# Kernel optimization log

Measured on AMD Instinct MI355X. Metric: run time of the kernel, lower is better.

## Reference

```python
import jax, jax.numpy as jnp
import numpy as np

B, C_IN, C_OUT, H, W = 64, 1024, 1024, 16, 16
HEADS, C_RED = 8, 512  # reduced_ch = 1024 // 2
N = H * W
EPS = 1e-5  # BatchNorm eps (eval mode, running stats)
NEG_SLOPE = 0.2  # PyG GATConv default leaky_relu slope


def build_grid_edge_index(P, Pw):
    # 4-neighbor grid + one self-loop per node, directed [2, E]
    edges = []
    for i in range(P):
        for j in range(Pw):
            u = i * Pw + j
            if i - 1 >= 0: edges.append([u, u - Pw])
            if i + 1 < P:  edges.append([u, u + Pw])
            if j - 1 >= 0: edges.append([u, u - 1])
            if j + 1 < Pw: edges.append([u, u + 1])
            edges.append([u, u])
    return jnp.asarray(np.array(edges, dtype=np.int32).T)


def setup_inputs() -> dict:
    key = jax.random.key(0)
    ks = jax.random.split(key, 10)
    x = jax.random.normal(ks[0], (B, C_IN, H, W), jnp.float32)
    w_reduce = jax.random.normal(ks[1], (C_RED, C_IN), jnp.float32) * 0.02
    g_red = jnp.ones((C_RED,), jnp.float32); b_red = jnp.zeros((C_RED,), jnp.float32)
    m_red = jax.random.normal(ks[2], (C_RED,), jnp.float32) * 0.1
    v_red = jax.random.uniform(ks[3], (C_RED,), jnp.float32) + 0.5
    w_gat = jax.random.normal(ks[4], (C_RED, HEADS * C_RED), jnp.float32) * 0.02
    att_src = jax.random.normal(ks[5], (HEADS, C_RED), jnp.float32) * 0.1
    att_dst = jax.random.normal(ks[6], (HEADS, C_RED), jnp.float32) * 0.1
    gat_bias = jnp.zeros((C_RED,), jnp.float32)
    w_restore = jax.random.normal(ks[7], (C_OUT, C_RED), jnp.float32) * 0.02
    g_res = jnp.ones((C_OUT,), jnp.float32); b_res = jnp.zeros((C_OUT,), jnp.float32)
    m_res = jax.random.normal(ks[8], (C_OUT,), jnp.float32) * 0.1
    v_res = jax.random.uniform(ks[9], (C_OUT,), jnp.float32) + 0.5
    edge_index = build_grid_edge_index(H, W)
    return dict(x=x, w_reduce=w_reduce, g_red=g_red, b_red=b_red, m_red=m_red, v_red=v_red,
                w_gat=w_gat, att_src=att_src, att_dst=att_dst, gat_bias=gat_bias,
                w_restore=w_restore, g_res=g_res, b_res=b_res, m_res=m_res, v_res=v_res,
                edge_index=edge_index)


def _bn(x, g, b, m, v):  # channel-last, eval mode
    return (x - m) * (g * jax.lax.rsqrt(v + EPS)) + b


def reference(x, w_reduce, g_red, b_red, m_red, v_red, w_gat, att_src, att_dst,
              gat_bias, w_restore, g_res, b_res, m_res, v_res, edge_index):
    xh = jnp.transpose(x, (0, 2, 3, 1))                 # [B,H,W,C_in] NHWC
    res = xh                                            # identity residual (C_in == C_out)
    xr = jax.nn.relu(_bn(xh @ w_reduce.T, g_red, b_red, m_red, v_red))  # [B,H,W,C_red]
    nodes = xr.reshape(B, N, C_RED)                     # per-sample grid graph nodes

    # --- GATConv (heads=HEADS, concat=False), batched over B ---
    xp = (nodes @ w_gat).reshape(B, N, HEADS, C_RED)    # projected per-head features
    a_src = jnp.einsum('bnhc,hc->bnh', xp, att_src)
    a_dst = jnp.einsum('bnhc,hc->bnh', xp, att_dst)
    src, dst = edge_index[0], edge_index[1]
    logits = jax.nn.leaky_relu(a_src[:, src] + a_dst[:, dst], NEG_SLOPE)  # [B,E,HEADS]
    seg_max = jax.vmap(lambda a: jax.ops.segment_max(a, dst, num_segments=N))(logits)
    e = jnp.exp(logits - seg_max[:, dst])
    seg_sum = jax.vmap(lambda a: jax.ops.segment_sum(a, dst, num_segments=N))(e)
    alpha = e / seg_sum[:, dst]                          # softmax over incoming edges
    msg = alpha[..., None] * xp[:, src]                  # [B,E,HEADS,C_red]
    agg = jax.vmap(lambda m_: jax.ops.segment_sum(m_, dst, num_segments=N))(msg)
    gat_out = agg.mean(axis=2) + gat_bias                # concat=False -> head mean, [B,N,C_red]

    out = gat_out.reshape(B, H, W, C_RED) @ w_restore.T  # 1x1 restore conv
    out = _bn(out, g_res, b_res, m_res, v_res)
    out = jax.nn.relu(out + res)
    return jnp.transpose(out, (0, 3, 1, 2))              # [B,C_out,H,W]
```

## Files before the change

### kernel.cpp

```cpp
#include <hip/hip_runtime.h>


typedef unsigned short u16;
typedef __attribute__((ext_vector_type(4))) unsigned short u16x4;
typedef __attribute__((ext_vector_type(8))) unsigned short u16x8;
typedef __attribute__((ext_vector_type(8))) __bf16 bf16x8;
typedef __attribute__((ext_vector_type(2))) __bf16 bf16x2;
typedef __attribute__((ext_vector_type(4))) float f32x4;

#if defined(__has_builtin)
#if __has_builtin(__builtin_amdgcn_fdot2_f32_bf16)
#define HAVE_DOT2 1
#endif
#endif

#define B_    64
#define CIN   1024
#define CRED  512
#define COUT  1024
#define NPIX  256
#define HEADS 8
#define KGAT  4096
#define MTOT  16384
#define EPSB  1e-5f

__device__ __forceinline__ float b2f(u16 u) {
  union { unsigned u; float f; } c; c.u = ((unsigned)u) << 16; return c.f;
}
__device__ __forceinline__ u16 f2b(float f) {
  union { float f; unsigned u; } c; c.f = f;
  unsigned r = (c.u + 0x7FFFu + ((c.u >> 16) & 1u)) >> 16;
  return (u16)r;
}

__device__ __forceinline__ void gload_lds16(const void* g, void* lds) {
  __builtin_amdgcn_global_load_lds(
      (const __attribute__((address_space(1))) void*)g,
      (__attribute__((address_space(3))) void*)lds, 16, 0, 0);
}

union U8u {
  u16x8 v;
  bf16x2 p[4];
};

__global__ __launch_bounds__(256) void alphapre_kernel(
    const float* __restrict__ a_all, u16* __restrict__ alf_g)
{
  const int nh = blockIdx.x * 256 + threadIdx.x;
  const int ng = nh >> 3, h = nh & 7;
  const int n = ng & 255;
  const size_t nbase = (size_t)(ng >> 8) * NPIX;
  const int gi = n >> 4, gj = n & 15;
  int vv[5];
  vv[0] = n;
  vv[1] = (gi > 0)  ? n - 16 : -1;
  vv[2] = (gi < 15) ? n + 16 : -1;
  vv[3] = (gj > 0)  ? n - 1  : -1;
  vv[4] = (gj < 15) ? n + 1  : -1;
  const float* a_src = a_all;
  const float* a_dst = a_all + (size_t)MTOT * HEADS;
  const float ad = a_dst[(nbase + n) * HEADS + h];
  float l[5]; float mx = -1e30f;
#pragma unroll
  for (int e = 0; e < 5; ++e) {
    if (vv[e] >= 0) {
      const float xx = a_src[(nbase + vv[e]) * HEADS + h] + ad;
      l[e] = xx > 0.f ? xx : 0.2f * xx;
      mx = fmaxf(mx, l[e]);
    } else l[e] = -1e30f;
  }
  float s = 0.f, ee[5];
#pragma unroll
  for (int e = 0; e < 5; ++e) {
    ee[e] = (vv[e] >= 0) ? __expf(l[e] - mx) : 0.f;
    s += ee[e];
  }
  const float inv = 0.125f / s;
#pragma unroll
  for (int e = 0; e < 5; ++e)
    alf_g[(size_t)ng * 40 + e * 8 + h] = f2b(ee[e] * inv);
}

__global__ __launch_bounds__(512, 4) void gemmf2_kernel(
    const u16* __restrict__ A, const u16* __restrict__ Btp,
    const u16* __restrict__ alf_g, const float* __restrict__ gat_bias,
    u16* __restrict__ gat)
{
  extern __shared__ u16 lds[];
  u16* Ys = lds;

  const int tid = threadIdx.x;
  const int wave = tid >> 6, lane = tid & 63;
  const int wm = wave >> 1, wn = wave & 1;
  const int l15 = lane & 15, l4 = lane >> 4;

  const int raw = blockIdx.x;
  const int lin = (raw & 7) * 256 + (raw >> 3);
  const int img = lin >> 5;
  const int ntile = lin & 31;
  const int n0 = ntile * 128;
  const int jbg = ntile * 16;
  const size_t nbase = (size_t)img * NPIX;

  int offA[2], dstA[2];
#pragma unroll
  for (int i = 0; i < 2; ++i) {
    const int f = i * 512 + tid;
    const int r = f >> 2;
    const int kb = (f & 3) ^ ((r >> 1) & 3);
    offA[i] = r * 512 + kb * 8;
    dstA[i] = (i * 512 + wave * 64) * 8;
  }
  const int rB = tid >> 2;
  const int kbB = (tid & 3) ^ ((rB >> 1) & 3);
  const int offB = rB * 512 + kbB * 8;
  const int dstB = wave * 64 * 8;

  const u16* gA = A + (size_t)img * 256 * 512;
  const u16* gB = Btp + (size_t)n0 * 512;

  auto stage = [&](int t) {
    const int d = (t & 1) * 12288;
    gload_lds16(gA + t * 32 + offA[0], &lds[d + dstA[0]]);
    gload_lds16(gA + t * 32 + offA[1], &lds[d + dstA[1]]);
    gload_lds16(gB + t * 32 + offB, &lds[d + 8192 + dstB]);
  };

  f32x4 acc[4][4];
#pragma unroll
  for (int i = 0; i < 4; ++i)
#pragma unroll
    for (int j = 0; j < 4; ++j) acc[i][j] = f32x4{0.f, 0.f, 0.f, 0.f};

  const int kq = (l4 ^ ((l15 >> 1) & 3)) * 8;
  const int aBase = (wm * 64 + l15) * 32 + kq;
  const int bBase = 8192 + (wn * 64 + l15) * 32 + kq;

  stage(0);

  for (int t = 0; t < 16; ++t) {
    asm volatile("s_waitcnt vmcnt(0)" ::: "memory");
    __builtin_amdgcn_s_barrier();
    const int d = (t & 1) * 12288;
    bf16x8 af[4], bfr[4];
#pragma unroll
    for (int f = 0; f < 4; ++f) {
      af[f]  = *(const bf16x8*)&lds[d + aBase + f * 512];
      bfr[f] = *(const bf16x8*)&lds[d + bBase + f * 512];
    }
    if (t < 15) stage(t + 1);
    __builtin_amdgcn_s_setprio(1);
#pragma unroll
    for (int fm = 0; fm < 4; ++fm)
#pragma unroll
      for (int fn = 0; fn < 4; ++fn)
        acc[fm][fn] = __builtin_amdgcn_mfma_f32_16x16x32_bf16(
            bfr[fn], af[fm], acc[fm][fn], 0, 0, 0);
    __builtin_amdgcn_s_setprio(0);
  }
  __syncthreads();

#pragma unroll
  for (int fm = 0; fm < 4; ++fm) {
    const int nloc = wm * 64 + fm * 16 + l15;
#pragma unroll
    for (int fn = 0; fn < 4; ++fn) {
      const int cloc = wn * 64 + fn * 16 + l4 * 4;
      u16x4 ov;
#pragma unroll
      for (int r = 0; r < 4; ++r) ov[r] = f2b(acc[fm][fn][r]);
      *(u16x4*)&Ys[nloc * 136 + cloc] = ov;
    }
  }
  __syncthreads();

  const int n = tid >> 1, half = tid & 1;
  const int gi = n >> 4, gj = n & 15;
  int vv[5];
  vv[0] = n;
  vv[1] = (gi > 0)  ? n - 16 : n;
  vv[2] = (gi < 15) ? n + 16 : n;
  vv[3] = (gj > 0)  ? n - 1  : n;
  vv[4] = (gj < 15) ? n + 1  : n;
  U8u au[5];
  {
    const u16* ag = alf_g + (nbase + n) * 40;
#pragma unroll
    for (int e = 0; e < 5; ++e) au[e].v = *(const u16x8*)&ag[e * 8];
  }
  float o[8];
  {
    const int jb = jbg + half * 8;
    const float4 b0 = *(const float4*)&gat_bias[jb];
    const float4 b1 = *(const float4*)&gat_bias[jb + 4];
    o[0] = b0.x; o[1] = b0.y; o[2] = b0.z; o[3] = b0.w;
    o[4] = b1.x; o[5] = b1.y; o[6] = b1.z; o[7] = b1.w;
  }
#pragma unroll
  for (int e = 0; e < 5; ++e) {
    const u16* yrow = &Ys[vv[e] * 136 + half * 64];
#if defined(HAVE_DOT2)
#pragma unroll
    for (int k = 0; k < 8; ++k) {
      U8u yu;
      yu.v = *(const u16x8*)&yrow[k * 8];
      float s = o[k];
      s = __builtin_amdgcn_fdot2_f32_bf16(yu.p[0], au[e].p[0], s, false);
      s = __builtin_amdgcn_fdot2_f32_bf16(yu.p[1], au[e].p[1], s, false);
      s = __builtin_amdgcn_fdot2_f32_bf16(yu.p[2], au[e].p[2], s, false);
      s = __builtin_amdgcn_fdot2_f32_bf16(yu.p[3], au[e].p[3], s, false);
      o[k] = s;
    }
#else
    float a8[8];
#pragma unroll
    for (int h = 0; h < 8; ++h) a8[h] = b2f(au[e].v[h]);
#pragma unroll
    for (int k = 0; k < 8; ++k) {
      const u16x8 yv = *(const u16x8*)&yrow[k * 8];
#pragma unroll
      for (int h = 0; h < 8; ++h) o[k] += a8[h] * b2f(yv[h]);
    }
#endif
  }
  u16x8 ov;
#pragma unroll
  for (int k = 0; k < 8; ++k) ov[k] = f2b(o[k]);
  *(u16x8*)&gat[(nbase + n) * (size_t)CRED + jbg + half * 8] = ov;
}

__global__ __launch_bounds__(512, 4) void gemm_res3_kernel(
    const u16* __restrict__ A, const u16* __restrict__ Bt,
    float* __restrict__ out32,
    const float* __restrict__ pg, const float* __restrict__ pb,
    const float* __restrict__ pm, const float* __restrict__ pv,
    const float* __restrict__ auxf)
{
  extern __shared__ u16 lds[];
  const int tid = threadIdx.x;
  const int wave = tid >> 6, lane = tid & 63;
  const int wm = wave >> 1, wn = wave & 1;
  const int l15 = lane & 15, l4 = lane >> 4;

  const int raw = blockIdx.x;
  const int lin = (raw & 7) * 64 + (raw >> 3);
  const int m0 = (lin >> 3) * 256;
  const int n0 = (lin & 7) * 128;

  int offA[2], dstA[2];
#pragma unroll
  for (int i = 0; i < 2; ++i) {
    const int f = i * 512 + tid;
    const int r = f >> 2;
    const int kb = (f & 3) ^ ((r >> 1) & 3);
    offA[i] = r * 512 + kb * 8;
    dstA[i] = (i * 512 + wave * 64) * 8;
  }
  const int rB = tid >> 2;
  const int kbB = (tid & 3) ^ ((rB >> 1) & 3);
  const int offB = rB * 512 + kbB * 8;
  const int dstB = wave * 64 * 8;

  const u16* gA = A + (size_t)m0 * 512;
  const u16* gB = Bt + (size_t)n0 * 512;

  auto stage = [&](int t) {
    const int d = (t & 1) * 12288;
    gload_lds16(gA + t * 32 + offA[0], &lds[d + dstA[0]]);
    gload_lds16(gA + t * 32 + offA[1], &lds[d + dstA[1]]);
    gload_lds16(gB + t * 32 + offB, &lds[d + 8192 + dstB]);
  };

  f32x4 acc[4][4];
#pragma unroll
  for (int i = 0; i < 4; ++i)
#pragma unroll
    for (int j = 0; j < 4; ++j) acc[i][j] = f32x4{0.f, 0.f, 0.f, 0.f};

  const int kq = (l4 ^ ((l15 >> 1) & 3)) * 8;
  const int aBase = (wm * 64 + l15) * 32 + kq;
  const int bBase = 8192 + (wn * 64 + l15) * 32 + kq;

  stage(0);

  for (int t = 0; t < 16; ++t) {
    asm volatile("s_waitcnt vmcnt(0)" ::: "memory");
    __builtin_amdgcn_s_barrier();
    const int d = (t & 1) * 12288;
    bf16x8 af[4], bfr[4];
#pragma unroll
    for (int f = 0; f < 4; ++f) {
      af[f]  = *(const bf16x8*)&lds[d + aBase + f * 512];
      bfr[f] = *(const bf16x8*)&lds[d + bBase + f * 512];
    }
    if (t < 15) stage(t + 1);
    __builtin_amdgcn_s_setprio(1);
#pragma unroll
    for (int fm = 0; fm < 4; ++fm)
#pragma unroll
      for (int fn = 0; fn < 4; ++fn)
        acc[fm][fn] = __builtin_amdgcn_mfma_f32_16x16x32_bf16(
            af[fm], bfr[fn], acc[fm][fn], 0, 0, 0);
    __builtin_amdgcn_s_setprio(0);
  }

  const int rowb = m0 + wm * 64 + l4 * 4;
#pragma unroll
  for (int fn = 0; fn < 4; ++fn) {
    const int col = n0 + wn * 64 + fn * 16 + l15;
    const float sc = pg[col] * rsqrtf(pv[col] + EPSB);
    const float off = pb[col] - pm[col] * sc;
#pragma unroll
    for (int fm = 0; fm < 4; ++fm) {
      const int row = rowb + fm * 16;
      const int bimg = row >> 8, p0 = row & 255;
      const size_t oa = (size_t)bimg * (COUT * NPIX) + (size_t)col * NPIX + p0;
      const float4 rv = *(const float4*)&auxf[oa];
      float4 ov;
      ov.x = fmaxf(acc[fm][fn][0] * sc + off + rv.x, 0.f);
      ov.y = fmaxf(acc[fm][fn][1] * sc + off + rv.y, 0.f);
      ov.z = fmaxf(acc[fm][fn][2] * sc + off + rv.z, 0.f);
      ov.w = fmaxf(acc[fm][fn][3] * sc + off + rv.w, 0.f);
      *(float4*)&out32[oa] = ov;
    }
  }
}

__global__ __launch_bounds__(256) void wgatp_kernel(
    const float* __restrict__ w_gat, u16* __restrict__ out)
{
  __shared__ float tile[64][65];
  const int cb = blockIdx.x;
  const int kb = blockIdx.y;
  const int t = threadIdx.x;
  const int jl = t & 7, h = (t >> 3) & 7, k4 = t >> 6;
#pragma unroll
  for (int i = 0; i < 16; ++i) {
    const int kl = k4 * 16 + i;
    tile[kl][jl * 8 + h] =
        w_gat[(size_t)(kb * 64 + kl) * KGAT + h * 512 + cb * 8 + jl];
  }
  __syncthreads();
#pragma unroll
  for (int i = 0; i < 4; ++i) {
    const int idx = i * 256 + t;
    const int cl = idx >> 4;
    const int kq = (idx & 15) * 4;
    u16x4 ov;
#pragma unroll
    for (int q = 0; q < 4; ++q) ov[q] = f2b(tile[kq + q][cl]);
    *(u16x4*)&out[(size_t)(cb * 64 + cl) * CRED + kb * 64 + kq] = ov;
  }
}

__global__ __launch_bounds__(256, 2) void gemm_redf_kernel(
    const float* __restrict__ x, const u16* __restrict__ Bt,
    u16* __restrict__ out16,
    const float* __restrict__ pg, const float* __restrict__ pb,
    const float* __restrict__ pm, const float* __restrict__ pv)
{
  __shared__ u16 As[64 * 32];
  __shared__ u16 Bs[128 * 32];
  const int tid = threadIdx.x;
  const int wave = tid >> 6, lane = tid & 63;
  const int gx = gridDim.x;
  const int nwg = gx * gridDim.y;
  int lin = blockIdx.y * gx + blockIdx.x;
  lin = (lin & 7) * (nwg >> 3) + (lin >> 3);
  const int m0 = (lin / gx) * 64, n0 = (lin % gx) * 128;
  const int bimg = m0 >> 8, p0 = m0 & 255;

  const float* xsrc = x + (size_t)bimg * CIN * NPIX + p0 + lane;

  int offB[2], dstB[2];
#pragma unroll
  for (int i = 0; i < 2; ++i) {
    const int f = i * 256 + tid;
    const int r = f >> 2;
    const int kb = (f & 3) ^ ((r >> 1) & 3);
    offB[i] = r * CIN + kb * 8;
    dstB[i] = (i * 256 + wave * 64) * 8;
  }
  const u16* gB = Bt + (size_t)n0 * CIN;

  const int aWr = (lane * 4 + (wave ^ ((lane >> 1) & 3))) * 8;

  f32x4 acc[2][4];
#pragma unroll
  for (int i = 0; i < 2; ++i)
#pragma unroll
    for (int j = 0; j < 4; ++j) acc[i][j] = f32x4{0.f, 0.f, 0.f, 0.f};

  const int wr = wave >> 1, wc = wave & 1;
  const int l15 = lane & 15, l4 = lane >> 4;
  const int kq = (l4 ^ ((l15 >> 1) & 3)) * 8;

  float av[8];
#pragma unroll
  for (int j = 0; j < 8; ++j) av[j] = xsrc[(wave * 8 + j) * NPIX];

  for (int kt = 0; kt < CIN; kt += 32) {
    u16x8 pvv;
#pragma unroll
    for (int j = 0; j < 8; ++j) pvv[j] = f2b(av[j]);
    *(u16x8*)&As[aWr] = pvv;
    gload_lds16(gB + kt + offB[0], &Bs[dstB[0]]);
    gload_lds16(gB + kt + offB[1], &Bs[dstB[1]]);
    __syncthreads();
    if (kt + 32 < CIN) {
#pragma unroll
      for (int j = 0; j < 8; ++j)
        av[j] = xsrc[(kt + 32 + wave * 8 + j) * NPIX];
    }
    bf16x8 af[2], bfr[4];
#pragma unroll
    for (int f = 0; f < 2; ++f)
      af[f] = *(const bf16x8*)&As[(wr * 32 + f * 16 + l15) * 32 + kq];
#pragma unroll
    for (int f = 0; f < 4; ++f)
      bfr[f] = *(const bf16x8*)&Bs[(wc * 64 + f * 16 + l15) * 32 + kq];
#pragma unroll
    for (int fm = 0; fm < 2; ++fm)
#pragma unroll
      for (int fn = 0; fn < 4; ++fn)
        acc[fm][fn] = __builtin_amdgcn_mfma_f32_16x16x32_bf16(
            af[fm], bfr[fn], acc[fm][fn], 0, 0, 0);
    __syncthreads();
  }

  const int rowb = m0 + wr * 32 + (lane >> 4) * 4;
#pragma unroll
  for (int fn = 0; fn < 4; ++fn) {
    const int col = n0 + wc * 64 + fn * 16 + l15;
    const float sc = pg[col] * rsqrtf(pv[col] + EPSB);
    const float off = pb[col] - pm[col] * sc;
#pragma unroll
    for (int fm = 0; fm < 2; ++fm) {
      const int row = rowb + fm * 16;
#pragma unroll
      for (int r = 0; r < 4; ++r) {
        const float y = fmaxf(acc[fm][fn][r] * sc + off, 0.f);
        out16[(size_t)(row + r) * CRED + col] = f2b(y);
      }
    }
  }
}

__global__ __launch_bounds__(256) void cvt2_kernel(
    const float* __restrict__ s0, u16* __restrict__ d0,
    const float* __restrict__ s1, u16* __restrict__ d1, int half)
{
  const int bi = blockIdx.x;
  const float* src = (bi < half) ? s0 : s1;
  u16* dst = (bi < half) ? d0 : d1;
  const int i = ((bi < half ? bi : bi - half) * 256 + threadIdx.x) * 8;
  const float4 a = *(const float4*)&src[i];
  const float4 b = *(const float4*)&src[i + 4];
  u16x8 o;
  o[0] = f2b(a.x); o[1] = f2b(a.y); o[2] = f2b(a.z); o[3] = f2b(a.w);
  o[4] = f2b(b.x); o[5] = f2b(b.y); o[6] = f2b(b.z); o[7] = f2b(b.w);
  *(u16x8*)&dst[i] = o;
}

__global__ __launch_bounds__(128) void attproj_kernel(
    const float* __restrict__ w_gat, const float* __restrict__ att_src,
    const float* __restrict__ att_dst, float* __restrict__ P)
{
  __shared__ float av[CRED];
  const int bi = blockIdx.x;
  const int sh = bi & 15, q = bi >> 4;
  const int s = sh >> 3, h = sh & 7;
  const float* att = (s == 0) ? att_src : att_dst;
  for (int t = threadIdx.x; t < CRED; t += 128) av[t] = att[h * CRED + t];
  __syncthreads();
  const int c = q * 128 + threadIdx.x;
  const float* wrow = w_gat + (size_t)c * KGAT + h * CRED;
  float acc = 0.f;
  for (int j = 0; j < CRED; j += 4) {
    const float4 w = *(const float4*)&wrow[j];
    acc += w.x * av[j] + w.y * av[j + 1] + w.z * av[j + 2] + w.w * av[j + 3];
  }
  P[(size_t)sh * CRED + c] = acc;
}

__global__ __launch_bounds__(256) void att_kernel(
    const u16* __restrict__ xr, const float* __restrict__ P,
    float* __restrict__ a_all)
{
  const int wave = threadIdx.x >> 6, lane = threadIdx.x & 63;
  const int m = blockIdx.x * 4 + wave;
  const int sh = lane & 15, q = lane >> 4;
  const u16* xp = xr + (size_t)m * CRED + q * 128;
  const float* Pp = P + (size_t)sh * CRED + q * 128;
  float s = 0.f;
#pragma unroll
  for (int c = 0; c < 128; c += 8) {
    u16x8 xv = *(const u16x8*)&xp[c];
#pragma unroll
    for (int t = 0; t < 8; ++t) s += b2f(xv[t]) * Pp[c + t];
  }
  s += __shfl_xor(s, 16);
  s += __shfl_xor(s, 32);
  if (q == 0)
    a_all[(size_t)(sh >> 3) * MTOT * HEADS + (size_t)m * HEADS + (sh & 7)] = s;
}

extern "C" void kernel_launch(void* const* d_in, const int* in_sizes, int n_in,
                              void* d_out, int out_size, void* d_ws, size_t ws_size,
                              hipStream_t stream)
{
  const float* x         = (const float*)d_in[0];
  const float* w_reduce  = (const float*)d_in[1];
  const float* g_red     = (const float*)d_in[2];
  const float* b_red     = (const float*)d_in[3];
  const float* m_red     = (const float*)d_in[4];
  const float* v_red     = (const float*)d_in[5];
  const float* w_gat     = (const float*)d_in[6];
  const float* att_src   = (const float*)d_in[7];
  const float* att_dst   = (const float*)d_in[8];
  const float* gat_bias  = (const float*)d_in[9];
  const float* w_restore = (const float*)d_in[10];
  const float* g_res     = (const float*)d_in[11];
  const float* b_res     = (const float*)d_in[12];
  const float* m_res     = (const float*)d_in[13];
  const float* v_res     = (const float*)d_in[14];

  constexpr size_t SZ_XR   = (size_t)MTOT * CRED * 2;
  constexpr size_t SZ_GAT  = SZ_XR;
  constexpr size_t SZ_WGT  = (size_t)KGAT * CRED * 2;
  constexpr size_t SZ_WRD  = (size_t)CRED * CIN * 2;
  constexpr size_t SZ_WRS  = (size_t)COUT * CRED * 2;
  constexpr size_t SZ_P    = (size_t)16 * CRED * 4;
  constexpr size_t SZ_AALL = (size_t)2 * MTOT * HEADS * 4;
  char* ws = (char*)d_ws;
  u16*   xr     = (u16*)ws;
  u16*   gat    = (u16*)(ws + SZ_XR);
  u16*   WgT2p  = (u16*)(ws + SZ_XR + SZ_GAT);
  u16*   wred_b = (u16*)(ws + SZ_XR + SZ_GAT + SZ_WGT);
  u16*   wres_b = (u16*)(ws + SZ_XR + SZ_GAT + SZ_WGT + SZ_WRD);
  float* P      = (float*)(ws + SZ_XR + SZ_GAT + SZ_WGT + SZ_WRD + SZ_WRS);
  float* a_all  = (float*)(ws + SZ_XR + SZ_GAT + SZ_WGT + SZ_WRD + SZ_WRS + SZ_P);
  u16*   alf_g  = (u16*)(ws + SZ_XR + SZ_GAT + SZ_WGT + SZ_WRD + SZ_WRS + SZ_P + SZ_AALL);
  float* outp   = (float*)d_out;

  hipFuncSetAttribute((const void*)gemmf2_kernel,
                      hipFuncAttributeMaxDynamicSharedMemorySize, 69632);
  hipFuncSetAttribute((const void*)gemm_res3_kernel,
                      hipFuncAttributeMaxDynamicSharedMemorySize, 49152);

  wgatp_kernel<<<dim3(64, 8), 256, 0, stream>>>(w_gat, WgT2p);
  cvt2_kernel<<<512, 256, 0, stream>>>(
      w_reduce, wred_b, w_restore, wres_b, 256);
  gemm_redf_kernel<<<dim3(4, 256), 256, 0, stream>>>(
      x, wred_b, xr, g_red, b_red, m_red, v_red);
  attproj_kernel<<<64, 128, 0, stream>>>(w_gat, att_src, att_dst, P);
  att_kernel<<<MTOT / 4, 256, 0, stream>>>(xr, P, a_all);
  alphapre_kernel<<<512, 256, 0, stream>>>(a_all, alf_g);
  gemmf2_kernel<<<2048, 512, 69632, stream>>>(
      xr, WgT2p, alf_g, gat_bias, gat);
  gemm_res3_kernel<<<512, 512, 49152, stream>>>(
      gat, wres_b, outp, g_res, b_res, m_res, v_res, x);
  (void)in_sizes; (void)n_in; (void)out_size; (void)ws_size;
}
```

Baseline: 234.7 us.

## Double-buffer LDS tiles in reduce GEMM and raise occupancy target

Converts the reduce-conv GEMM main loop to ping-pong LDS buffers. The next tile's global loads are issued before the MFMAs and the converted A tile is written into the other buffer afterwards, which cuts the loop to one barrier per iteration. It also raises the launch-bounds occupancy hint from 2 to 4 and brackets the MFMA block with s_setprio. The risks are doubled LDS use, which can limit occupancy, and tighter register limits from the higher hint, which could cause spills.

```diff
diff --git a/kernel.cpp b/kernel.cpp
--- a/kernel.cpp
+++ b/kernel.cpp
@@ -354,14 +354,14 @@
   }
 }
 
-__global__ __launch_bounds__(256, 2) void gemm_redf_kernel(
+__global__ __launch_bounds__(256, 4) void gemm_redf_kernel(
     const float* __restrict__ x, const u16* __restrict__ Bt,
     u16* __restrict__ out16,
     const float* __restrict__ pg, const float* __restrict__ pb,
     const float* __restrict__ pm, const float* __restrict__ pv)
 {
-  __shared__ u16 As[64 * 32];
-  __shared__ u16 Bs[128 * 32];
+  __shared__ u16 As[2][64 * 32];
+  __shared__ u16 Bs[2][128 * 32];
   const int tid = threadIdx.x;
   const int wave = tid >> 6, lane = tid & 63;
   const int gx = gridDim.x;
@@ -399,34 +399,47 @@
   float av[8];
 #pragma unroll
   for (int j = 0; j < 8; ++j) av[j] = xsrc[(wave * 8 + j) * NPIX];
-
-  for (int kt = 0; kt < CIN; kt += 32) {
+  {
     u16x8 pvv;
 #pragma unroll
     for (int j = 0; j < 8; ++j) pvv[j] = f2b(av[j]);
-    *(u16x8*)&As[aWr] = pvv;
-    gload_lds16(gB + kt + offB[0], &Bs[dstB[0]]);
-    gload_lds16(gB + kt + offB[1], &Bs[dstB[1]]);
+    *(u16x8*)&As[0][aWr] = pvv;
+  }
+  gload_lds16(gB + offB[0], &Bs[0][dstB[0]]);
+  gload_lds16(gB + offB[1], &Bs[0][dstB[1]]);
+
+  for (int t = 0; t < 32; ++t) {
     __syncthreads();
-    if (kt + 32 < CIN) {
+    const int cur = t & 1, nxt = cur ^ 1;
+    const int ktn = (t + 1) * 32;
+    if (t < 31) {
 #pragma unroll
       for (int j = 0; j < 8; ++j)
-        av[j] = xsrc[(kt + 32 + wave * 8 + j) * NPIX];
+        av[j] = xsrc[(ktn + wave * 8 + j) * NPIX];
+      gload_lds16(gB + ktn + offB[0], &Bs[nxt][dstB[0]]);
+      gload_lds16(gB + ktn + offB[1], &Bs[nxt][dstB[1]]);
     }
     bf16x8 af[2], bfr[4];
 #pragma unroll
     for (int f = 0; f < 2; ++f)
-      af[f] = *(const bf16x8*)&As[(wr * 32 + f * 16 + l15) * 32 + kq];
+      af[f] = *(const bf16x8*)&As[cur][(wr * 32 + f * 16 + l15) * 32 + kq];
 #pragma unroll
     for (int f = 0; f < 4; ++f)
-      bfr[f] = *(const bf16x8*)&Bs[(wc * 64 + f * 16 + l15) * 32 + kq];
+      bfr[f] = *(const bf16x8*)&Bs[cur][(wc * 64 + f * 16 + l15) * 32 + kq];
+    __builtin_amdgcn_s_setprio(1);
 #pragma unroll
     for (int fm = 0; fm < 2; ++fm)
 #pragma unroll
       for (int fn = 0; fn < 4; ++fn)
         acc[fm][fn] = __builtin_amdgcn_mfma_f32_16x16x32_bf16(
             af[fm], bfr[fn], acc[fm][fn], 0, 0, 0);
-    __syncthreads();
+    __builtin_amdgcn_s_setprio(0);
+    if (t < 31) {
+      u16x8 pvv;
+#pragma unroll
+      for (int j = 0; j < 8; ++j) pvv[j] = f2b(av[j]);
+      *(u16x8*)&As[nxt][aWr] = pvv;
+    }
   }
 
   const int rowb = m0 + wr * 32 + (lane >> 4) * 4;
```

New measurement: 234.8 us. No clear change (+0.0%).
